# Kernel tuning notes

Measured on AMD Instinct MI355X. Metric: run time of the kernel, lower is better.

The kernel has to match this reference:

```python
import jax, jax.numpy as jnp
import numpy as np

EMBED_DIM = 1024
NUM_HEADS = 16
HEAD_DIM = EMBED_DIM // NUM_HEADS


def setup_inputs() -> dict:
    key = jax.random.key(0)
    ks = jax.random.split(key, 9)
    s = 1.0 / np.sqrt(EMBED_DIM)
    X = jax.random.normal(ks[0], (4, 2048, EMBED_DIM), dtype=jnp.float32)
    # Linear weights stored as [in, out] for x @ W + b
    Wq = jax.random.uniform(ks[1], (EMBED_DIM, EMBED_DIM), jnp.float32, -s, s)
    bq = jax.random.uniform(ks[2], (EMBED_DIM,), jnp.float32, -s, s)
    Wk = jax.random.uniform(ks[3], (EMBED_DIM, EMBED_DIM), jnp.float32, -s, s)
    bk = jax.random.uniform(ks[4], (EMBED_DIM,), jnp.float32, -s, s)
    Wv = jax.random.uniform(ks[5], (EMBED_DIM, EMBED_DIM), jnp.float32, -s, s)
    bv = jax.random.uniform(ks[6], (EMBED_DIM,), jnp.float32, -s, s)
    Wo = jax.random.uniform(ks[7], (EMBED_DIM, EMBED_DIM), jnp.float32, -s, s)
    bo = jax.random.uniform(ks[8], (EMBED_DIM,), jnp.float32, -s, s)
    return {"X": X, "Wq": Wq, "bq": bq, "Wk": Wk, "bk": bk,
            "Wv": Wv, "bv": bv, "Wo": Wo, "bo": bo}


def reference(X, Wq, bq, Wk, bk, Wv, bv, Wo, bo):
    B, S, _ = X.shape
    def split_heads(t):  # [B,S,E] -> [B,H,S,D]
        return t.reshape(B, S, NUM_HEADS, HEAD_DIM).transpose(0, 2, 1, 3)
    Q = split_heads(X @ Wq + bq)
    K = split_heads(X @ Wk + bk)
    V = split_heads(X @ Wv + bv)
    scale = 1.0 / np.sqrt(HEAD_DIM).astype(np.float32)
    scores = jnp.einsum('bhqd,bhkd->bhqk', Q, K) * scale
    probs = jax.nn.softmax(scores, axis=-1)
    attn = jnp.einsum('bhqk,bhkd->bhqd', probs, V)  # [B,H,S,D]
    combined = attn.transpose(0, 2, 1, 3).reshape(B, S, EMBED_DIM)
    return combined @ Wo + bo
```

## Files before the change

kernel.cpp:

```cpp
#include <hip/hip_runtime.h>
#include <hip/hip_bf16.h>

#define EMBED 1024
#define NHEADS 16
#define HDIM 64
#define SEQ 2048
#define BATCH 4
#define ROWS (BATCH * SEQ)

typedef __attribute__((ext_vector_type(8))) short bf16x8;
typedef __attribute__((ext_vector_type(4))) float f32x4;
typedef __attribute__((ext_vector_type(2))) float f32x2;
typedef __attribute__((ext_vector_type(16))) float f32x16;
typedef __attribute__((ext_vector_type(4))) unsigned int u32x4;
typedef __attribute__((ext_vector_type(2))) unsigned int u32x2;
typedef __attribute__((ext_vector_type(2))) int i32x2;
typedef unsigned int u32;

#define SL2E 0.18033688011112042f

__device__ __forceinline__ short f2bf(float f) {
    u32 u = __builtin_bit_cast(u32, f) + 0x8000u;
    return (short)(u >> 16);
}

__device__ __forceinline__ u32 pkbf(float a, float b) {
    u32 ua = __builtin_bit_cast(u32, a) + 0x8000u;
    u32 ub = __builtin_bit_cast(u32, b) + 0x8000u;
    return __builtin_amdgcn_perm(ua, ub, 0x03020706u);
}

__device__ __forceinline__ float fexp2(float x) {
#if __has_builtin(__builtin_amdgcn_exp2f)
    return __builtin_amdgcn_exp2f(x);
#else
    return exp2f(x);
#endif
}

__device__ __forceinline__ void async16(const void* g, void* l) {
    __builtin_amdgcn_global_load_lds((const __attribute__((address_space(1))) u32*)g,
                                     (__attribute__((address_space(3))) u32*)l, 16, 0, 0);
}

__global__ __launch_bounds__(256) void convert_f32_bf16(const float* __restrict__ in,
                                                        short* __restrict__ out) {
    int i = (blockIdx.x * 256 + threadIdx.x) * 4;
    float4 v = *(const float4*)&in[i];
    u32x2 o = { pkbf(v.x, v.y), pkbf(v.z, v.w) };
    *(u32x2*)&out[i] = o;
}

__global__ __launch_bounds__(256) void transpose_w4(const float* __restrict__ W0,
                                                    const float* __restrict__ W1,
                                                    const float* __restrict__ W2,
                                                    const float* __restrict__ W3,
                                                    short* __restrict__ T0,
                                                    short* __restrict__ T1,
                                                    short* __restrict__ T2,
                                                    short* __restrict__ T3) {
    const int z = blockIdx.z;
    const float* W = (z == 0) ? W0 : (z == 1) ? W1 : (z == 2) ? W2 : W3;
    short* WT = (z == 0) ? T0 : (z == 1) ? T1 : (z == 2) ? T2 : T3;
    const float sc = (z == 0) ? SL2E : 1.0f;
    __shared__ float T[64][65];
    const int k0 = blockIdx.y * 64, n0 = blockIdx.x * 64;
    const int rr = threadIdx.x >> 4, cc = (threadIdx.x & 15) * 4;
    #pragma unroll
    for (int p = 0; p < 4; ++p) {
        int r = p * 16 + rr;
        float4 v = *(const float4*)&W[(size_t)(k0 + r) * EMBED + n0 + cc];
        T[r][cc] = v.x * sc; T[r][cc + 1] = v.y * sc; T[r][cc + 2] = v.z * sc; T[r][cc + 3] = v.w * sc;
    }
    __syncthreads();
    #pragma unroll
    for (int p = 0; p < 4; ++p) {
        int r = p * 16 + rr;
        u32x2 o = { pkbf(T[cc][r], T[cc + 1][r]), pkbf(T[cc + 2][r], T[cc + 3][r]) };
        *(u32x2*)&WT[(size_t)(n0 + r) * EMBED + k0 + cc] = o;
    }
}

__global__ __launch_bounds__(512, 2) void gemm_p128(const short* __restrict__ A,
                                                    const short* __restrict__ BT,
                                                    const float* __restrict__ b0,
                                                    const float* __restrict__ b1,
                                                    const float* __restrict__ b2,
                                                    void* __restrict__ C0,
                                                    void* __restrict__ C1,
                                                    void* __restrict__ C2,
                                                    int mode) {
    __shared__ short As[2][8192];
    __shared__ short Bs[2][16384];
    const int tid = threadIdx.x;
    const int lane = tid & 63;
    const int wid = tid >> 6;
    const int c16 = lane & 15, quad = lane >> 4, sw = c16 & 7;
    const int wm = wid >> 2, wn = wid & 3;
    const int gx = gridDim.x;
    const int hid = blockIdx.y * gx + blockIdx.x;
    const int cpx = (gx * gridDim.y) >> 3;
    const int tle = (hid & 7) * cpx + (hid >> 3);
    const int bx = tle % gx, by = tle / gx;
    const int rowblk = by * 128, colblk = bx * 256;

    const int r0 = tid >> 3;
    const int g0 = (tid & 7) ^ (r0 & 7);
    const short* aS0 = A + (size_t)(rowblk + r0) * EMBED + g0 * 8;
    const short* bS0 = BT + (size_t)(colblk + r0) * EMBED + g0 * 8;

#define STAGE_A(SBUF, V) do { \
    const short* _s = aS0 + (V) * 64; \
    async16(_s,         &As[SBUF][tid * 8]); \
    async16(_s + 65536, &As[SBUF][tid * 8 + 4096]); \
} while (0)
#define STAGE_B0(SBUF, V) do { \
    const short* _s = bS0 + (V) * 64; \
    async16(_s,         &Bs[SBUF][tid * 8]); \
    async16(_s + 65536, &Bs[SBUF][tid * 8 + 4096]); \
} while (0)
#define STAGE_B1(SBUF, V) do { \
    const short* _s = bS0 + 131072 + (V) * 64; \
    async16(_s,         &Bs[SBUF][tid * 8 + 8192]); \
    async16(_s + 65536, &Bs[SBUF][tid * 8 + 12288]); \
} while (0)

    f32x4 acc[4][4] = {};
    bf16x8 aU[2][2], bE[2][2], bO[2][2];

#define LDA(BUF, MH) do { \
    _Pragma("unroll") \
    for (int fm = 0; fm < 2; ++fm) { \
        const int row = wm * 64 + (MH) * 32 + fm * 16 + c16; \
        _Pragma("unroll") \
        for (int ks = 0; ks < 2; ++ks) \
            aU[fm][ks] = *(const bf16x8*)&As[BUF][row * 64 + ((ks * 4 + quad) ^ sw) * 8]; \
    } \
} while (0)
#define LDB(BUF, NH, DST) do { \
    _Pragma("unroll") \
    for (int fn = 0; fn < 2; ++fn) { \
        const int col = wn * 64 + (NH) * 32 + fn * 16 + c16; \
        _Pragma("unroll") \
        for (int ks = 0; ks < 2; ++ks) \
            DST[fn][ks] = *(const bf16x8*)&Bs[BUF][col * 64 + ((ks * 4 + quad) ^ sw) * 8]; \
    } \
} while (0)
#define MM(MB, NB, BM_) do { \
    _Pragma("unroll") \
    for (int fm = 0; fm < 2; ++fm) \
        _Pragma("unroll") \
        for (int fn = 0; fn < 2; ++fn) \
            _Pragma("unroll") \
            for (int ks = 0; ks < 2; ++ks) \
                acc[(MB) + fm][(NB) + fn] = \
                    __builtin_amdgcn_mfma_f32_16x16x32_bf16(aU[fm][ks], BM_[fn][ks], \
                        acc[(MB) + fm][(NB) + fn], 0, 0, 0); \
} while (0)
#define PH_MID() do { \
    __builtin_amdgcn_s_barrier(); \
    asm volatile("s_waitcnt lgkmcnt(0)" ::: "memory"); \
    __builtin_amdgcn_s_setprio(1); \
} while (0)
#define PH_END(VM) do { \
    __builtin_amdgcn_s_setprio(0); \
    if (VM) asm volatile("s_waitcnt vmcnt(6)" ::: "memory"); \
    __builtin_amdgcn_s_barrier(); \
} while (0)

    STAGE_B0(0, 0); STAGE_A(0, 0); STAGE_B1(0, 0);
    STAGE_B0(1, 1); STAGE_A(1, 1); STAGE_B1(1, 1);
    asm volatile("s_waitcnt vmcnt(6)" ::: "memory");
    __builtin_amdgcn_s_barrier();

    #pragma unroll 1
    for (int it = 0; it < 8; ++it) {
        const int u = 2 * it;
        const int v2 = (u + 2) & 15, v3 = (u + 3) & 15;
        LDA(0, 0); LDB(0, 0, bE);                     PH_MID(); MM(0, 0, bE); PH_END(0);
        LDB(0, 1, bO);            STAGE_B0(0, v2);    PH_MID(); MM(0, 2, bO); PH_END(0);
        LDA(0, 1);                STAGE_B1(0, v2);    PH_MID(); MM(2, 2, bO); PH_END(0);
                 STAGE_A(0, v2);     PH_MID(); MM(2, 0, bE); PH_END(1);
        LDA(1, 0); LDB(1, 0, bE);                     PH_MID(); MM(0, 0, bE); PH_END(0);
        LDB(1, 1, bO);            STAGE_B0(1, v3);    PH_MID(); MM(0, 2, bO); PH_END(0);
        LDA(1, 1);                STAGE_B1(1, v3);    PH_MID(); MM(2, 2, bO); PH_END(0);
                 STAGE_A(1, v3);     PH_MID(); MM(2, 0, bE); PH_END(1);
    }

    asm volatile("s_waitcnt vmcnt(0)" ::: "memory");

    const int rb0 = rowblk + wm * 64 + quad * 4;
    const int cb0 = wn * 64 + c16;
    if (mode == 0) {
        const int z = colblk >> 10;
        const int cm = colblk & 1023;
        const float* bias = (z == 0) ? b0 : (z == 1) ? b1 : b2;
        if (z == 2) {
            short* Vt = (short*)C2;
            #pragma unroll
            for (int m = 0; m < 4; ++m) {
                const int row = rb0 + (m >> 1) * 32 + (m & 1) * 16;
                const int b = row >> 11, s = row & 2047;
                #pragma unroll
                for (int n = 0; n < 4; ++n) {
                    const int cv = cm + cb0 + (n >> 1) * 32 + (n & 1) * 16;
                    const int head = cv >> 6, d = cv & 63;
                    const float bv = bias[cv];
                    u32x2 o = { pkbf(acc[m][n][0] + bv, acc[m][n][1] + bv),
                                pkbf(acc[m][n][2] + bv, acc[m][n][3] + bv) };
                    *(u32x2*)&Vt[((size_t)(b * NHEADS + head) * HDIM + d) * SEQ + s] = o;
                }
            }
        } else {
            short* Cq = (short*)((z == 0) ? C0 : C1);
            const float bsc = (z == 0) ? SL2E : 1.0f;
            #pragma unroll
            for (int m = 0; m < 4; ++m) {
                const int row = rb0 + (m >> 1) * 32 + (m & 1) * 16;
                #pragma unroll
                for (int n = 0; n < 4; ++n) {
                    const int col = cm + cb0 + (n >> 1) * 32 + (n & 1) * 16;
                    const float bv = bias[col] * bsc;
                    #pragma unroll
                    for (int r = 0; r < 4; ++r)
                        Cq[(size_t)(row + r) * EMBED + col] = f2bf(acc[m][n][r] + bv);
                }
            }
        }
    } else {
        float* Co = (float*)C0;
        #pragma unroll
        for (int m = 0; m < 4; ++m) {
            const int row = rb0 + (m >> 1) * 32 + (m & 1) * 16;
            #pragma unroll
            for (int n = 0; n < 4; ++n) {
                const int col = colblk + cb0 + (n >> 1) * 32 + (n & 1) * 16;
                const float bv = b0[col];
                #pragma unroll
                for (int r = 0; r < 4; ++r)
                    Co[(size_t)(row + r) * EMBED + col] = acc[m][n][r] + bv;
            }
        }
    }
#undef PH_END
#undef PH_MID
#undef MM
#undef LDB
#undef LDA
#undef STAGE_B1
#undef STAGE_B0
#undef STAGE_A
}

__global__ __launch_bounds__(256, 3) void attn_mfma(const short* __restrict__ Qb,
                                                    const short* __restrict__ Kb,
                                                    const short* __restrict__ Vt,
                                                    short* __restrict__ Ob) {
    __shared__ short SH[16384];
    const int tid = threadIdx.x;
    const int wave = tid >> 6, lane = tid & 63;
    const int l31 = lane & 31, h = lane >> 5;
    const int swz = l31 & 7;
    const int hid = blockIdx.y * 16 + blockIdx.x;
    const int tle = (hid & 7) * 128 + (hid >> 3);
    const int qb = tle & 15, bh = tle >> 4;
    const int b = bh >> 4, hd = bh & 15;
    const size_t base = (size_t)b * SEQ * EMBED + (size_t)hd * HDIM;
    const size_t vbase = (size_t)bh * HDIM * SEQ;
    const int q0 = qb * 128;

    bf16x8 qf[4];
    #pragma unroll
    for (int ks = 0; ks < 4; ++ks)
        qf[ks] = *(const bf16x8*)&Qb[base + (size_t)(q0 + wave * 32 + l31) * EMBED + ks * 16 + h * 8];

    const short* kp[2];
    const short* vp[2];
    int ldofs[2];
    #pragma unroll
    for (int it = 0; it < 2; ++it) {
        int ci = (it * 4 + wave) * 64 + lane;
        int row = ci >> 3, g = (ci & 7) ^ (row & 7);
        kp[it] = Kb + base + (size_t)row * EMBED + g * 8;
        vp[it] = Vt + vbase + (size_t)row * SEQ + g * 8;
        ldofs[it] = (it * 4 + wave) * 512;
    }

#define STAGE_K(J) do { \
    async16(kp[0], &SH[(J) * 4096 + ldofs[0]]); \
    async16(kp[1], &SH[(J) * 4096 + ldofs[1]]); \
    kp[0] += 64 * EMBED; kp[1] += 64 * EMBED; \
} while (0)
#define STAGE_V(J) do { \
    async16(vp[0], &SH[8192 + (J) * 4096 + ldofs[0]]); \
    async16(vp[1], &SH[8192 + (J) * 4096 + ldofs[1]]); \
    vp[0] += 64; vp[1] += 64; \
} while (0)
#define QK_INTO(ST, J) do { \
    _Pragma("unroll") \
    for (int _z = 0; _z < 16; ++_z) { ST[0][_z] = 0.0f; ST[1][_z] = 0.0f; } \
    __builtin_amdgcn_s_setprio(1); \
    _Pragma("unroll") \
    for (int nt = 0; nt < 2; ++nt) \
        _Pragma("unroll") \
        for (int ks = 0; ks < 4; ++ks) { \
            bf16x8 ak = *(const bf16x8*)&SH[(J) * 4096 + (nt * 32 + l31) * 64 + ((ks * 2 + h) ^ swz) * 8]; \
            ST[nt] = __builtin_amdgcn_mfma_f32_32x32x16_bf16(ak, qf[ks], ST[nt], 0, 0, 0); \
        } \
    __builtin_amdgcn_s_setprio(0); \
} while (0)

    f32x16 O[2] = {};
    f32x16 stA[2], stB[2];
    f32x2 ls = {0.0f, 0.0f};

    STAGE_K(0); STAGE_V(0); STAGE_K(1);
    asm volatile("s_waitcnt vmcnt(0)" ::: "memory");
    __builtin_amdgcn_s_barrier();
    QK_INTO(stA, 0);
    __builtin_amdgcn_s_barrier();

#define ATT_BODY(CUR, NXT, STC, STN, DO_K, DO_V, DO_QK) do { \
    if (DO_K) STAGE_K(CUR); \
    if (DO_V) STAGE_V(NXT); \
    if (DO_QK) QK_INTO(STN, NXT); \
    u32 pk[2][8]; \
    _Pragma("unroll") \
    for (int nt = 0; nt < 2; ++nt) \
        _Pragma("unroll") \
        for (int i = 0; i < 8; ++i) { \
            float e0 = fexp2(STC[nt][2 * i]), e1 = fexp2(STC[nt][2 * i + 1]); \
            f32x2 e = { e0, e1 }; \
            ls += e; \
            pk[nt][i] = pkbf(e0, e1); \
        } \
    __builtin_amdgcn_s_setprio(1); \
    _Pragma("unroll") \
    for (int ks = 0; ks < 4; ++ks) { \
        const int nt = ks >> 1, bs = (ks & 1) * 4; \
        u32x4 fr; \
        i32x2 sA = __builtin_amdgcn_permlane32_swap((int)pk[nt][bs + 0], (int)pk[nt][bs + 2], false, false); \
        i32x2 sB = __builtin_amdgcn_permlane32_swap((int)pk[nt][bs + 1], (int)pk[nt][bs + 3], false, false); \
        fr.x = (u32)sA.x; fr.y = (u32)sB.x; fr.z = (u32)sA.y; fr.w = (u32)sB.y; \
        bf16x8 pf = __builtin_bit_cast(bf16x8, fr); \
        _Pragma("unroll") \
        for (int mt = 0; mt < 2; ++mt) { \
            bf16x8 vf = *(const bf16x8*)&SH[8192 + (CUR) * 4096 + (mt * 32 + l31) * 64 + ((ks * 2 + h) ^ swz) * 8]; \
            O[mt] = __builtin_amdgcn_mfma_f32_32x32x16_bf16(vf, pf, O[mt], 0, 0, 0); \
        } \
    } \
    __builtin_amdgcn_s_setprio(0); \
    asm volatile("s_waitcnt vmcnt(0)" ::: "memory"); \
    __builtin_amdgcn_s_barrier(); \
} while (0)

    #pragma unroll 1
    for (int t = 0; t < 30; t += 2) {
        ATT_BODY(0, 1, stA, stB, 1, 1, 1);
        ATT_BODY(1, 0, stB, stA, 1, 1, 1);
    }
    ATT_BODY(0, 1, stA, stB, 0, 1, 1);
    ATT_BODY(1, 0, stB, stA, 0, 0, 0);

#undef ATT_BODY
#undef QK_INTO
#undef STAGE_V
#undef STAGE_K

    float lsum = ls.x + ls.y;
    lsum += __shfl_xor(lsum, 32);
    float inv = 1.0f / lsum;

    const int wbase = wave * 2048;
    #pragma unroll
    for (int mt = 0; mt < 2; ++mt)
        #pragma unroll
        for (int m = 0; m < 4; ++m) {
            u32x2 wv;
            wv.x = pkbf(O[mt][4 * m + 0] * inv, O[mt][4 * m + 1] * inv);
            wv.y = pkbf(O[mt][4 * m + 2] * inv, O[mt][4 * m + 3] * inv);
            int u = mt * 8 + 2 * m + h;
            int su = u ^ ((l31 & 7) << 1);
            *(u32x2*)&SH[wbase + l31 * 64 + su * 4] = wv;
        }
    __syncthreads();
    #pragma unroll
    for (int p = 0; p < 4; ++p) {
        int ci = p * 256 + tid;
        int wq = ci >> 8, rem = ci & 255;
        int r = rem >> 3, cch = rem & 7;
        int su = (2 * cch) ^ ((r & 7) << 1);
        bf16x8 val = *(const bf16x8*)&SH[wq * 2048 + r * 64 + su * 4];
        *(bf16x8*)&Ob[base + (size_t)(q0 + wq * 32 + r) * EMBED + cch * 8] = val;
    }
}

extern "C" void kernel_launch(void* const* d_in, const int* in_sizes, int n_in,
                              void* d_out, int out_size, void* d_ws, size_t ws_size,
                              hipStream_t stream)
{
    const float* X  = (const float*)d_in[0];
    const float* Wq = (const float*)d_in[1];
    const float* bq = (const float*)d_in[2];
    const float* Wk = (const float*)d_in[3];
    const float* bk = (const float*)d_in[4];
    const float* Wv = (const float*)d_in[5];
    const float* bv = (const float*)d_in[6];
    const float* Wo = (const float*)d_in[7];
    const float* bo = (const float*)d_in[8];
    float* out = (float*)d_out;

    const size_t NE = (size_t)ROWS * EMBED;
    short* Xbf = (short*)d_ws;
    short* Qb  = Xbf + NE;
    short* Kb  = Qb + NE;
    short* Vtb = Kb + NE;
    short* WqT = Vtb + NE;
    short* WkT = WqT + (size_t)EMBED * EMBED;
    short* WvT = WkT + (size_t)EMBED * EMBED;
    short* WoT = WvT + (size_t)EMBED * EMBED;

    convert_f32_bf16<<<(ROWS * EMBED) / 1024, 256, 0, stream>>>(X, Xbf);
    dim3 gw(16, 16, 4);
    transpose_w4<<<gw, 256, 0, stream>>>(Wq, Wk, Wv, Wo, WqT, WkT, WvT, WoT);

    dim3 gq(12, 64, 1);
    gemm_p128<<<gq, 512, 0, stream>>>(Xbf, WqT, bq, bk, bv, Qb, Kb, Vtb, 0);

    dim3 gt(SEQ / 128, BATCH * NHEADS);
    attn_mfma<<<gt, 256, 0, stream>>>(Qb, Kb, Vtb, Qb);

    dim3 gg(4, 64, 1);
    gemm_p128<<<gg, 512, 0, stream>>>(Qb, WoT, bo, bo, bo, out, out, out, 1);
}
```

Before: 270.0 us.

## Drop QK software pipelining in attention to cut registers and raise occupancy

The attention loop no longer computes the next tile's QK scores one step ahead into a second score buffer. Each 64-key tile now stages K and V together, then per 32-key half computes scores, exponentiates them and accumulates into O. This frees the double score accumulators so launch bounds can go from 3 to 4 blocks per CU. The cost is that the in-wave overlap of QK MFMA with the exp/PV work is lost, and the kernel relies on more resident waves to hide that latency.

```diff
diff --git a/kernel.cpp b/kernel.cpp
--- a/kernel.cpp
+++ b/kernel.cpp
@@ -252,7 +252,7 @@
 #undef STAGE_A
 }
 
-__global__ __launch_bounds__(256, 3) void attn_mfma(const short* __restrict__ Qb,
+__global__ __launch_bounds__(256, 4) void attn_mfma(const short* __restrict__ Qb,
                                                     const short* __restrict__ Kb,
                                                     const short* __restrict__ Vt,
                                                     short* __restrict__ Ob) {
@@ -286,86 +286,74 @@
         ldofs[it] = (it * 4 + wave) * 512;
     }
 
-#define STAGE_K(J) do { \
+#define STAGE_KV(J) do { \
     async16(kp[0], &SH[(J) * 4096 + ldofs[0]]); \
     async16(kp[1], &SH[(J) * 4096 + ldofs[1]]); \
-    kp[0] += 64 * EMBED; kp[1] += 64 * EMBED; \
-} while (0)
-#define STAGE_V(J) do { \
     async16(vp[0], &SH[8192 + (J) * 4096 + ldofs[0]]); \
     async16(vp[1], &SH[8192 + (J) * 4096 + ldofs[1]]); \
+    kp[0] += 64 * EMBED; kp[1] += 64 * EMBED; \
     vp[0] += 64; vp[1] += 64; \
 } while (0)
-#define QK_INTO(ST, J) do { \
-    _Pragma("unroll") \
-    for (int _z = 0; _z < 16; ++_z) { ST[0][_z] = 0.0f; ST[1][_z] = 0.0f; } \
-    __builtin_amdgcn_s_setprio(1); \
-    _Pragma("unroll") \
-    for (int nt = 0; nt < 2; ++nt) \
-        _Pragma("unroll") \
-        for (int ks = 0; ks < 4; ++ks) { \
-            bf16x8 ak = *(const bf16x8*)&SH[(J) * 4096 + (nt * 32 + l31) * 64 + ((ks * 2 + h) ^ swz) * 8]; \
-            ST[nt] = __builtin_amdgcn_mfma_f32_32x32x16_bf16(ak, qf[ks], ST[nt], 0, 0, 0); \
-        } \
-    __builtin_amdgcn_s_setprio(0); \
-} while (0)
 
     f32x16 O[2] = {};
-    f32x16 stA[2], stB[2];
     f32x2 ls = {0.0f, 0.0f};
 
-    STAGE_K(0); STAGE_V(0); STAGE_K(1);
+    STAGE_KV(0);
     asm volatile("s_waitcnt vmcnt(0)" ::: "memory");
     __builtin_amdgcn_s_barrier();
-    QK_INTO(stA, 0);
-    __builtin_amdgcn_s_barrier();
-
-#define ATT_BODY(CUR, NXT, STC, STN, DO_K, DO_V, DO_QK) do { \
-    if (DO_K) STAGE_K(CUR); \
-    if (DO_V) STAGE_V(NXT); \
-    if (DO_QK) QK_INTO(STN, NXT); \
-    u32 pk[2][8]; \
+
+#define ATT_TILE(CUR, NXT, DO_STAGE) do { \
+    if (DO_STAGE) STAGE_KV(NXT); \
     _Pragma("unroll") \
-    for (int nt = 0; nt < 2; ++nt) \
+    for (int nt = 0; nt < 2; ++nt) { \
+        f32x16 st = {0.0f, 0.0f, 0.0f, 0.0f, 0.0f, 0.0f, 0.0f, 0.0f, \
+                     0.0f, 0.0f, 0.0f, 0.0f, 0.0f, 0.0f, 0.0f, 0.0f}; \
+        __builtin_amdgcn_s_setprio(1); \
+        _Pragma("unroll") \
+        for (int ks = 0; ks < 4; ++ks) { \
+            bf16x8 ak = *(const bf16x8*)&SH[(CUR) * 4096 + (nt * 32 + l31) * 64 + ((ks * 2 + h) ^ swz) * 8]; \
+            st = __builtin_amdgcn_mfma_f32_32x32x16_bf16(ak, qf[ks], st, 0, 0, 0); \
+        } \
+        __builtin_amdgcn_s_setprio(0); \
+        u32 pk[8]; \
         _Pragma("unroll") \
         for (int i = 0; i < 8; ++i) { \
-            float e0 = fexp2(STC[nt][2 * i]), e1 = fexp2(STC[nt][2 * i + 1]); \
+            float e0 = fexp2(st[2 * i]), e1 = fexp2(st[2 * i + 1]); \
             f32x2 e = { e0, e1 }; \
             ls += e; \
-            pk[nt][i] = pkbf(e0, e1); \
+            pk[i] = pkbf(e0, e1); \
         } \
-    __builtin_amdgcn_s_setprio(1); \
-    _Pragma("unroll") \
-    for (int ks = 0; ks < 4; ++ks) { \
-        const int nt = ks >> 1, bs = (ks & 1) * 4; \
-        u32x4 fr; \
-        i32x2 sA = __builtin_amdgcn_permlane32_swap((int)pk[nt][bs + 0], (int)pk[nt][bs + 2], false, false); \
-        i32x2 sB = __builtin_amdgcn_permlane32_swap((int)pk[nt][bs + 1], (int)pk[nt][bs + 3], false, false); \
-        fr.x = (u32)sA.x; fr.y = (u32)sB.x; fr.z = (u32)sA.y; fr.w = (u32)sB.y; \
-        bf16x8 pf = __builtin_bit_cast(bf16x8, fr); \
-        _Pragma("unroll") \
-        for (int mt = 0; mt < 2; ++mt) { \
-            bf16x8 vf = *(const bf16x8*)&SH[8192 + (CUR) * 4096 + (mt * 32 + l31) * 64 + ((ks * 2 + h) ^ swz) * 8]; \
-            O[mt] = __builtin_amdgcn_mfma_f32_32x32x16_bf16(vf, pf, O[mt], 0, 0, 0); \
+        __builtin_amdgcn_s_setprio(1); \
+        _Pragma("unroll") \
+        for (int kk = 0; kk < 2; ++kk) { \
+            const int ks = nt * 2 + kk, bs = kk * 4; \
+            u32x4 fr; \
+            i32x2 sA = __builtin_amdgcn_permlane32_swap((int)pk[bs + 0], (int)pk[bs + 2], false, false); \
+            i32x2 sB = __builtin_amdgcn_permlane32_swap((int)pk[bs + 1], (int)pk[bs + 3], false, false); \
+            fr.x = (u32)sA.x; fr.y = (u32)sB.x; fr.z = (u32)sA.y; fr.w = (u32)sB.y; \
+            bf16x8 pf = __builtin_bit_cast(bf16x8, fr); \
+            _Pragma("unroll") \
+            for (int mt = 0; mt < 2; ++mt) { \
+                bf16x8 vf = *(const bf16x8*)&SH[8192 + (CUR) * 4096 + (mt * 32 + l31) * 64 + ((ks * 2 + h) ^ swz) * 8]; \
+                O[mt] = __builtin_amdgcn_mfma_f32_32x32x16_bf16(vf, pf, O[mt], 0, 0, 0); \
+            } \
         } \
+        __builtin_amdgcn_s_setprio(0); \
     } \
-    __builtin_amdgcn_s_setprio(0); \
     asm volatile("s_waitcnt vmcnt(0)" ::: "memory"); \
     __builtin_amdgcn_s_barrier(); \
 } while (0)
 
     #pragma unroll 1
     for (int t = 0; t < 30; t += 2) {
-        ATT_BODY(0, 1, stA, stB, 1, 1, 1);
-        ATT_BODY(1, 0, stB, stA, 1, 1, 1);
-    }
-    ATT_BODY(0, 1, stA, stB, 0, 1, 1);
-    ATT_BODY(1, 0, stB, stA, 0, 0, 0);
-
-#undef ATT_BODY
-#undef QK_INTO
-#undef STAGE_V
-#undef STAGE_K
+        ATT_TILE(0, 1, 1);
+        ATT_TILE(1, 0, 1);
+    }
+    ATT_TILE(0, 1, 1);
+    ATT_TILE(1, 0, 0);
+
+#undef ATT_TILE
+#undef STAGE_KV
 
     float lsum = ls.x + ls.y;
     lsum += __shfl_xor(lsum, 32);
```

After: 259.4 us. -4.0%, faster.
